# Optimization experiments

Measured on AMD Instinct MI355X. Metric: run time of the kernel, lower is better.

## Reference

```python
import jax, jax.numpy as jnp
import numpy as np

B, S, H = 2, 2048, 2048
NH, NKV, HD = 16, 4, 128
GROUPS = NH // NKV
THETA = 10000.0
EPS = 1e-6


def setup_inputs() -> dict:
    key = jax.random.key(0)
    ks = jax.random.split(key, 6)
    scale = 0.02
    return {
        "hidden_states": jax.random.normal(ks[0], (B, S, H), jnp.float32),
        "wq": jax.random.normal(ks[1], (NH * HD, H), jnp.float32) * scale,
        "wk": jax.random.normal(ks[2], (NKV * HD, H), jnp.float32) * scale,
        "wv": jax.random.normal(ks[3], (NKV * HD, H), jnp.float32) * scale,
        "wo": jax.random.normal(ks[4], (H, NH * HD), jnp.float32) * scale,
        "q_norm_weight": jnp.ones((HD,), jnp.float32),
        "k_norm_weight": jnp.ones((HD,), jnp.float32),
    }


def _rope_tables(seq_len):
    inv_freq = 1.0 / (THETA ** (jnp.arange(0, HD, 2, dtype=jnp.float32) / HD))
    t = jnp.arange(seq_len, dtype=jnp.float32)
    freqs = jnp.outer(t, inv_freq)              # [S, HD/2]
    emb = jnp.concatenate([freqs, freqs], -1)   # [S, HD]
    return jnp.cos(emb), jnp.sin(emb)


def _rotate_half(x):
    x1, x2 = x[..., : HD // 2], x[..., HD // 2:]
    return jnp.concatenate([-x2, x1], -1)


def _rmsnorm(x, w):
    var = jnp.mean(jnp.square(x), axis=-1, keepdims=True)
    return x * jax.lax.rsqrt(var + EPS) * w


def reference(hidden_states, wq, wk, wv, wo, q_norm_weight, k_norm_weight):
    b, s, _ = hidden_states.shape
    q = (hidden_states @ wq.T).reshape(b, s, NH, HD).transpose(0, 2, 1, 3)    # [b,nh,s,d]
    k = (hidden_states @ wk.T).reshape(b, s, NKV, HD).transpose(0, 2, 1, 3)   # [b,nkv,s,d]
    v = (hidden_states @ wv.T).reshape(b, s, NKV, HD).transpose(0, 2, 1, 3)

    cos, sin = _rope_tables(s)                  # [s,d]
    q = q * cos + _rotate_half(q) * sin
    k = k * cos + _rotate_half(k) * sin

    # fused QK RMSNorm (applied inside fused_qknorm_flash_attention)
    q = _rmsnorm(q, q_norm_weight)
    k = _rmsnorm(k, k_norm_weight)

    # GQA: share each kv head across GROUPS query heads without materializing repeats
    qg = q.reshape(b, NKV, GROUPS, s, HD)
    scale = 1.0 / jnp.sqrt(jnp.float32(HD))
    scores = jnp.einsum('bhgqd,bhkd->bhgqk', qg, k) * scale   # [b,nkv,g,s,s]
    causal = jnp.tril(jnp.ones((s, s), bool))
    scores = jnp.where(causal, scores, jnp.finfo(scores.dtype).min)
    probs = jax.nn.softmax(scores, axis=-1)
    out = jnp.einsum('bhgqk,bhkd->bhgqd', probs, v)            # [b,nkv,g,s,d]
    out = out.reshape(b, NH, s, HD).transpose(0, 2, 1, 3).reshape(b, s, NH * HD)
    return out @ wo.T
```

## Files before the change

### kernel.cpp

```cpp
#include <hip/hip_runtime.h>
#include <math.h>

typedef __bf16 bf16;
typedef __bf16 bf16x8 __attribute__((ext_vector_type(8)));
typedef __bf16 bf16x4 __attribute__((ext_vector_type(4)));
typedef float f32x4 __attribute__((ext_vector_type(4)));
typedef unsigned int u32;

#define B_DIM 2
#define S_LEN 2048
#define H_DIM 2048
#define NH 16
#define NKV 4
#define HD 128

__device__ __forceinline__ void gl_lds16(const void* g, void* l) {
    __builtin_amdgcn_global_load_lds(
        (const __attribute__((address_space(1))) unsigned int*)g,
        (__attribute__((address_space(3))) unsigned int*)l, 16, 0, 0);
}

__device__ __forceinline__ void bar() {
    asm volatile("" ::: "memory");
    __builtin_amdgcn_s_barrier();
    asm volatile("" ::: "memory");
}

__global__ __launch_bounds__(256) void cast_all(const float* __restrict__ s0,
                                                const float* __restrict__ s1,
                                                const float* __restrict__ s2,
                                                const float* __restrict__ s3,
                                                const float* __restrict__ s4,
                                                bf16* __restrict__ dst) {
    const int i = blockIdx.x * 256 + threadIdx.x;
    const float* src;
    int off;
    if (i < 2097152)      { src = s0; off = 0; }
    else if (i < 3145728) { src = s1; off = 2097152; }
    else if (i < 3407872) { src = s2; off = 3145728; }
    else if (i < 3670016) { src = s3; off = 3407872; }
    else                  { src = s4; off = 3670016; }
    float4 f = ((const float4*)src)[i - off];
    bf16x4 o = { (bf16)f.x, (bf16)f.y, (bf16)f.z, (bf16)f.w };
    *(bf16x4*)(dst + (size_t)i * 4) = o;
}

template <typename OutT>
__global__ __launch_bounds__(512, 2) void gemm256(const bf16* __restrict__ A,
                                                  const bf16* __restrict__ Bt,
                                                  OutT* __restrict__ C,
                                                  int M, int N, int K) {
    __shared__ __align__(16) bf16 smem[65536];
    const int t = threadIdx.x, lane = t & 63, w = t >> 6;
    const int lr = lane & 15, quad = lane >> 4;
    const int nN = N >> 8;
    const int nwg = gridDim.x, chunk = nwg >> 3;
    const int bid = blockIdx.x;
    const int lid = (bid & 7) * chunk + (bid >> 3);
    const int m0 = (lid / nN) << 8, n0 = (lid % nN) << 8;
    const int mh_w = w >> 2;
    const int wn = (w & 3) << 6;
    const int nh_w = (w & 3) >> 1;
    const int rb = (w & 1) << 6;
    const int nK = K >> 6;

    const int ld0 = w * 2;
    const int lrow = lane >> 2;
    const int csrc = (lane & 3) ^ ((lane >> 3) & 3);
    const int swz = (lr >> 1) & 3;

    auto stA = [&](int ts, int mh) {
        if (ts < nK) {
            bf16* db = smem + (ts & 1) * 16384 + mh * 8192;
            const bf16* sp = A + (size_t)(m0 + mh * 128) * K + ts * 64;
#pragma unroll
            for (int i = 0; i < 2; i++) {
                const int ldi = ld0 + i, kb = ldi >> 3, rg = ldi & 7;
                gl_lds16(sp + (size_t)(rg * 16 + lrow) * K + kb * 32 + csrc * 8,
                         db + kb * 4096 + rg * 512);
            }
        }
    };
    auto stB = [&](int ts, int nh) {
        if (ts < nK) {
            bf16* db = smem + 32768 + (ts & 1) * 16384 + nh * 8192;
            const bf16* sp = Bt + (size_t)(n0 + nh * 128) * K + ts * 64;
#pragma unroll
            for (int i = 0; i < 2; i++) {
                const int ldi = ld0 + i, kb = ldi >> 3, rg = ldi & 7;
                gl_lds16(sp + (size_t)(rg * 16 + lrow) * K + kb * 32 + csrc * 8,
                         db + kb * 4096 + rg * 512);
            }
        }
    };

    f32x4 acc[8][4];
#pragma unroll
    for (int i = 0; i < 8; i++)
#pragma unroll
        for (int j = 0; j < 4; j++) acc[i][j] = (f32x4){0.f, 0.f, 0.f, 0.f};
    bf16x8 af[8], b0[4], b1[4];

    auto rdA = [&](int s, int fi0) {
        const bf16* bp = smem + s * 16384 + mh_w * 8192;
#pragma unroll
        for (int f = 0; f < 4; f++)
#pragma unroll
            for (int ks = 0; ks < 2; ks++)
                af[f * 2 + ks] = *(const bf16x8*)(bp + ks * 4096 +
                                                  ((fi0 + f) * 16 + lr) * 32 + (quad ^ swz) * 8);
    };
    auto rdB = [&](int s, int fj0, bf16x8* dst) {
        const bf16* bp = smem + 32768 + s * 16384 + nh_w * 8192;
#pragma unroll
        for (int f = 0; f < 2; f++)
#pragma unroll
            for (int ks = 0; ks < 2; ks++)
                dst[f * 2 + ks] = *(const bf16x8*)(bp + ks * 4096 +
                                                   (rb + (fj0 + f) * 16 + lr) * 32 + (quad ^ swz) * 8);
    };
    auto mm16 = [&](int fi0, int fj0, bf16x8* bb) {
        __builtin_amdgcn_s_setprio(1);
#pragma unroll
        for (int f = 0; f < 4; f++)
#pragma unroll
            for (int g = 0; g < 2; g++)
#pragma unroll
                for (int ks = 0; ks < 2; ks++)
                    acc[fi0 + f][fj0 + g] = __builtin_amdgcn_mfma_f32_16x16x32_bf16(
                        af[f * 2 + ks], bb[g * 2 + ks], acc[fi0 + f][fj0 + g], 0, 0, 0);
        __builtin_amdgcn_s_setprio(0);
    };

    stA(0, 0); stA(0, 1); stB(0, 0); stB(0, 1); stA(1, 0);
    asm volatile("s_waitcnt vmcnt(2)" ::: "memory");
    bar();

    for (int ts = 0; ts < nK; ++ts) {
        const int s = ts & 1;
        rdA(s, 0); rdB(s, 0, b0);
        stA(ts + 1, 1);
        bar();
        mm16(0, 0, b0);
        bar();
        rdB(s, 2, b1);
        stB(ts + 1, 0);
        bar();
        mm16(0, 2, b1);
        bar();
        rdA(s, 4);
        stB(ts + 1, 1);
        bar();
        mm16(4, 2, b1);
        bar();
        rdB(s, 0, b0);
        stA(ts + 2, 0);
        bar();
        mm16(4, 0, b0);
        if (ts + 2 < nK) asm volatile("s_waitcnt vmcnt(2)" ::: "memory");
        else             asm volatile("s_waitcnt vmcnt(0)" ::: "memory");
        bar();
    }
#pragma unroll
    for (int fi = 0; fi < 8; fi++) {
        const int m = m0 + mh_w * 128 + fi * 16 + quad * 4;
#pragma unroll
        for (int fj = 0; fj < 4; fj++) {
            const int n = n0 + wn + fj * 16 + lr;
#pragma unroll
            for (int r = 0; r < 4; r++)
                C[(size_t)(m + r) * N + n] = (OutT)acc[fi][fj][r];
        }
    }
}

__global__ __launch_bounds__(512, 1) void gemm_pn(const bf16* __restrict__ A,
                                                  const bf16* __restrict__ Bt,
                                                  float* __restrict__ C,
                                                  int M, int N, int K) {
    __shared__ __align__(16) bf16 smem[49152];
    const int t = threadIdx.x, lane = t & 63, w = t >> 6;
    const int lr = lane & 15, quad = lane >> 4;
    const int nN = N >> 7;
    const int nwg = gridDim.x, chunk = nwg >> 3;
    const int bid = blockIdx.x;
    const int lid = (bid & 7) * chunk + (bid >> 3);
    const int m0 = (lid / nN) << 8, n0 = (lid % nN) << 7;
    const int mh_w = w >> 2;
    const int wn = (w & 3) << 5;
    const int nK = K >> 6;

    const int ld0 = w * 2;
    const int lrow = lane >> 2;
    const int csrc = (lane & 3) ^ ((lane >> 3) & 3);
    const int swz = (lr >> 1) & 3;

    auto stA = [&](int ts, int mh) {
        if (ts < nK) {
            bf16* db = smem + (ts & 1) * 16384 + mh * 8192;
            const bf16* sp = A + (size_t)(m0 + mh * 128) * K + ts * 64;
#pragma unroll
            for (int i = 0; i < 2; i++) {
                const int ldi = ld0 + i, kb = ldi >> 3, rg = ldi & 7;
                gl_lds16(sp + (size_t)(rg * 16 + lrow) * K + kb * 32 + csrc * 8,
                         db + kb * 4096 + rg * 512);
            }
        }
    };
    auto stB1 = [&](int ts) {
        if (ts < nK) {
            bf16* db = smem + 32768 + (ts & 1) * 8192;
            const bf16* sp = Bt + (size_t)n0 * K + ts * 64;
#pragma unroll
            for (int i = 0; i < 2; i++) {
                const int ldi = ld0 + i, kb = ldi >> 3, rg = ldi & 7;
                gl_lds16(sp + (size_t)(rg * 16 + lrow) * K + kb * 32 + csrc * 8,
                         db + kb * 4096 + rg * 512);
            }
        }
    };

    f32x4 acc[8][2];
#pragma unroll
    for (int i = 0; i < 8; i++)
#pragma unroll
        for (int j = 0; j < 2; j++) acc[i][j] = (f32x4){0.f, 0.f, 0.f, 0.f};
    bf16x8 af[8], bf1[4];

    auto rdA = [&](int s, int fi0) {
        const bf16* bp = smem + s * 16384 + mh_w * 8192;
#pragma unroll
        for (int f = 0; f < 4; f++)
#pragma unroll
            for (int ks = 0; ks < 2; ks++)
                af[f * 2 + ks] = *(const bf16x8*)(bp + ks * 4096 +
                                                  ((fi0 + f) * 16 + lr) * 32 + (quad ^ swz) * 8);
    };
    auto rdB1 = [&](int s) {
        const bf16* bp = smem + 32768 + s * 8192;
#pragma unroll
        for (int f = 0; f < 2; f++)
#pragma unroll
            for (int ks = 0; ks < 2; ks++)
                bf1[f * 2 + ks] = *(const bf16x8*)(bp + ks * 4096 +
                                                   (wn + f * 16 + lr) * 32 + (quad ^ swz) * 8);
    };
    auto mm8 = [&](int fi0, int ks) {
        __builtin_amdgcn_s_setprio(1);
#pragma unroll
        for (int f = 0; f < 4; f++)
#pragma unroll
            for (int g = 0; g < 2; g++)
                acc[fi0 + f][g] = __builtin_amdgcn_mfma_f32_16x16x32_bf16(
                    af[f * 2 + ks], bf1[g * 2 + ks], acc[fi0 + f][g], 0, 0, 0);
        __builtin_amdgcn_s_setprio(0);
    };

    stA(0, 0); stA(0, 1); stB1(0);
    asm volatile("s_waitcnt vmcnt(0)" ::: "memory");
    bar();

    for (int ts = 0; ts < nK; ++ts) {
        const int s = ts & 1;
        rdA(s, 0); rdB1(s);
        stA(ts + 1, 0);
        bar();
        mm8(0, 0);
        bar();
        stA(ts + 1, 1);
        stB1(ts + 1);
        bar();
        mm8(0, 1);
        bar();
        rdA(s, 4);
        bar();
        mm8(4, 0);
        bar();
        mm8(4, 1);
        asm volatile("s_waitcnt vmcnt(0)" ::: "memory");
        bar();
    }
#pragma unroll
    for (int fi = 0; fi < 8; fi++) {
        const int m = m0 + mh_w * 128 + fi * 16 + quad * 4;
#pragma unroll
        for (int fj = 0; fj < 2; fj++) {
            const int n = n0 + wn + fj * 16 + lr;
#pragma unroll
            for (int r = 0; r < 4; r++)
                C[(size_t)(m + r) * N + n] = acc[fi][fj][r];
        }
    }
}

__global__ __launch_bounds__(256) void rope_rms(const bf16* __restrict__ qkv,
                                                const float* __restrict__ qw,
                                                const float* __restrict__ kw,
                                                bf16* __restrict__ qb,
                                                bf16* __restrict__ kb,
                                                bf16* __restrict__ vt) {
    const int tok = blockIdx.x;
    const int b = tok >> 11, s = tok & (S_LEN - 1);
    const int lane = threadIdx.x & 63, w = threadIdx.x >> 6;
    const bf16* row = qkv + (size_t)tok * 3072;
    const float inv = expf(-(float)lane * (9.210340371976184f / 64.f));
    const float ang = (float)s * inv;
    float s_, c_;
    sincosf(ang, &s_, &c_);
    const float wq1 = qw[lane], wq2 = qw[lane + 64];
    const float wk1 = kw[lane], wk2 = kw[lane + 64];
    for (int u = w; u < 24; u += 4) {
        if (u < 16) {
            const float x1 = (float)row[u * 128 + lane], x2 = (float)row[u * 128 + 64 + lane];
            float y1 = x1 * c_ - x2 * s_;
            float y2 = x2 * c_ + x1 * s_;
            float ss = y1 * y1 + y2 * y2;
#pragma unroll
            for (int m = 1; m < 64; m <<= 1) ss += __shfl_xor(ss, m);
            const float r = rsqrtf(ss * (1.f / 128.f) + 1e-6f);
            size_t o = ((size_t)(b * NH + u) * S_LEN + s) * HD;
            qb[o + lane]      = (bf16)(y1 * r * wq1);
            qb[o + 64 + lane] = (bf16)(y2 * r * wq2);
        } else if (u < 20) {
            const int kh = u - 16;
            const float x1 = (float)row[2048 + kh * 128 + lane], x2 = (float)row[2048 + kh * 128 + 64 + lane];
            float y1 = x1 * c_ - x2 * s_;
            float y2 = x2 * c_ + x1 * s_;
            float ss = y1 * y1 + y2 * y2;
#pragma unroll
            for (int m = 1; m < 64; m <<= 1) ss += __shfl_xor(ss, m);
            const float r = rsqrtf(ss * (1.f / 128.f) + 1e-6f);
            size_t base = (size_t)(b * NKV + kh) * 16 * 16384;
            kb[base + (size_t)(lane >> 3) * 16384 + s * 8 + (lane & 7)]       = (bf16)(y1 * r * wk1);
            kb[base + (size_t)(8 + (lane >> 3)) * 16384 + s * 8 + (lane & 7)] = (bf16)(y2 * r * wk2);
        } else {
            const int vh = u - 20;
            const float x1 = (float)row[2560 + vh * 128 + lane], x2 = (float)row[2560 + vh * 128 + 64 + lane];
            const int m = s & 31;
            const int gi = (s >> 5) * 4 + ((m & 15) >> 2);
            const int el = ((m >> 4) << 2) | (m & 3);
            size_t base = ((size_t)(b * NKV + vh) * 256 + gi) * 1024 + el;
            vt[base + (size_t)lane * 8]        = (bf16)x1;
            vt[base + (size_t)(lane + 64) * 8] = (bf16)x2;
        }
    }
}

__global__ __launch_bounds__(256, 2) void flash(const bf16* __restrict__ qg,
                                                const bf16* __restrict__ kg,
                                                const bf16* __restrict__ vg,
                                                bf16* __restrict__ attn,
                                                float* __restrict__ part_o,
                                                float* __restrict__ part_l) {
    static const unsigned char QT[22] = {9,8,15,15,7,14,14,13,13,6,12,12,11,11,5,10,10,4,3,2,1,0};
    static const unsigned char CK[22] = {2,2,0,1,2,0,1,0,1,2,0,1,0,1,2,0,1,2,2,2,2,2};
    const int idx = blockIdx.x;
    const int g = idx >> 5, hb = idx & 31;
    const int qt = QT[g], ck = CK[g];
    const int h = hb & 15, b = hb >> 4;
    const int kvh = h >> 2;
    const int ktBeg = (ck == 1) ? (qt + 1) : 0;
    const int ktEnd = (ck == 0) ? (qt + 1) : (2 * qt + 2);
    const bf16* qh = qg + (size_t)(b * NH + h) * S_LEN * HD;
    const bf16* kh = kg + (size_t)(b * NKV + kvh) * (16 * 16384);
    const bf16* vh = vg + (size_t)(b * NKV + kvh) * (256 * 1024);
    __shared__ __align__(16) bf16 Ks[2][16 * 512];
    __shared__ __align__(16) bf16 Vs[2][8 * 1024];
    const int t = threadIdx.x, lane = t & 63, w = t >> 6, lr = lane & 15, quad = lane >> 4;
    const int row0 = qt * 128 + w * 32;
    bf16x8 qf[2][4];
#pragma unroll
    for (int mg = 0; mg < 2; mg++)
#pragma unroll
        for (int c = 0; c < 4; c++)
            qf[mg][c] = *(const bf16x8*)(qh + (size_t)(row0 + mg * 16 + lr) * HD + c * 32 + quad * 8);
    f32x4 o[2][8];
    f32x4 lacc[2];
#pragma unroll
    for (int mg = 0; mg < 2; mg++) {
        lacc[mg] = (f32x4){0.f, 0.f, 0.f, 0.f};
#pragma unroll
        for (int j = 0; j < 8; j++) o[mg][j] = (f32x4){0.f, 0.f, 0.f, 0.f};
    }
    const bf16 one = (bf16)1.0f;
    const bf16x8 ones8 = {one, one, one, one, one, one, one, one};
    const float C1 = 0.12751744f;
    const float C2 = -17.3123405f;

    const bf16* kp[4];
    const bf16* vp[2];
#pragma unroll
    for (int i = 0; i < 4; i++) kp[i] = kh + (size_t)(w * 4 + i) * 16384 + lane * 8;
#pragma unroll
    for (int i = 0; i < 2; i++) vp[i] = vh + (size_t)(w * 2 + i) * 1024 + lane * 8;

    auto stage = [&](int kt_, int bi) {
        const size_t kb8 = (size_t)kt_ * 512;
#pragma unroll
        for (int i = 0; i < 4; i++)
            gl_lds16(kp[i] + kb8, &Ks[bi][(w * 4 + i) * 512]);
        const size_t vb = (size_t)kt_ * 8192;
#pragma unroll
        for (int i = 0; i < 2; i++) {
            gl_lds16(vp[i] + vb, &Vs[bi][(w * 2 + i) * 1024]);
            gl_lds16(vp[i] + vb + 512, &Vs[bi][(w * 2 + i) * 1024 + 512]);
        }
    };

    stage(ktBeg, 0);
    __syncthreads();
    int cur = 0;

    for (int kt = ktBeg; kt < ktEnd; ++kt) {
        const int kbase = kt * 64;
        if (kt + 1 < ktEnd) stage(kt + 1, cur ^ 1);
        f32x4 sacc[2][4];
#pragma unroll
        for (int mg = 0; mg < 2; mg++)
#pragma unroll
            for (int n = 0; n < 4; n++) sacc[mg][n] = (f32x4){0.f, 0.f, 0.f, 0.f};
        __builtin_amdgcn_s_setprio(1);
#pragma unroll
        for (int c = 0; c < 4; c++)
#pragma unroll
            for (int n = 0; n < 4; n++) {
                bf16x8 kf = *(const bf16x8*)&Ks[cur][(c * 4 + quad) * 512 + (n * 16 + lr) * 8];
                sacc[0][n] = __builtin_amdgcn_mfma_f32_16x16x32_bf16(kf, qf[0][c], sacc[0][n], 0, 0, 0);
                sacc[1][n] = __builtin_amdgcn_mfma_f32_16x16x32_bf16(kf, qf[1][c], sacc[1][n], 0, 0, 0);
            }
        __builtin_amdgcn_s_setprio(0);
        const bool diag = (kt >= 2 * qt);
        u32 pw[2][8];
#pragma unroll
        for (int mg = 0; mg < 2; mg++) {
            const int qrow = row0 + mg * 16 + lr;
#pragma unroll
            for (int n = 0; n < 4; n++) {
                float e0, e1, e2, e3;
                {
                    float ev0 = exp2f(fmaf(sacc[mg][n][0], C1, C2));
                    float ev1 = exp2f(fmaf(sacc[mg][n][1], C1, C2));
                    float ev2 = exp2f(fmaf(sacc[mg][n][2], C1, C2));
                    float ev3 = exp2f(fmaf(sacc[mg][n][3], C1, C2));
                    if (diag) {
                        const int key = kbase + n * 16 + quad * 4;
                        ev0 = (key + 0 <= qrow) ? ev0 : 0.f;
                        ev1 = (key + 1 <= qrow) ? ev1 : 0.f;
                        ev2 = (key + 2 <= qrow) ? ev2 : 0.f;
                        ev3 = (key + 3 <= qrow) ? ev3 : 0.f;
                    }
                    e0 = ev0; e1 = ev1; e2 = ev2; e3 = ev3;
                }
                asm("v_cvt_pk_bf16_f32 %0, %1, %2"
                    : "=v"(pw[mg][(n >> 1) * 4 + (n & 1) * 2 + 0]) : "v"(e0), "v"(e1));
                asm("v_cvt_pk_bf16_f32 %0, %1, %2"
                    : "=v"(pw[mg][(n >> 1) * 4 + (n & 1) * 2 + 1]) : "v"(e2), "v"(e3));
            }
        }
        __builtin_amdgcn_s_setprio(1);
#pragma unroll
        for (int k2 = 0; k2 < 2; k2++) {
            const bf16x8 p0 = *(const bf16x8*)&pw[0][k2 * 4];
            const bf16x8 p1 = *(const bf16x8*)&pw[1][k2 * 4];
#pragma unroll
            for (int j = 0; j < 8; j++) {
                bf16x8 vf = *(const bf16x8*)&Vs[cur][(k2 * 4 + quad) * 1024 + (j * 16 + lr) * 8];
                o[0][j] = __builtin_amdgcn_mfma_f32_16x16x32_bf16(vf, p0, o[0][j], 0, 0, 0);
                o[1][j] = __builtin_amdgcn_mfma_f32_16x16x32_bf16(vf, p1, o[1][j], 0, 0, 0);
            }
            lacc[0] = __builtin_amdgcn_mfma_f32_16x16x32_bf16(ones8, p0, lacc[0], 0, 0, 0);
            lacc[1] = __builtin_amdgcn_mfma_f32_16x16x32_bf16(ones8, p1, lacc[1], 0, 0, 0);
        }
        __builtin_amdgcn_s_setprio(0);
        __syncthreads();
        cur ^= 1;
    }
    if (ck == 2) {
#pragma unroll
        for (int mg = 0; mg < 2; mg++) {
            const float inv = 1.0f / lacc[mg][0];
            const int qrow = row0 + mg * 16 + lr;
            bf16* dst = attn + ((size_t)(b * S_LEN) + qrow) * (NH * HD) + h * HD + quad * 4;
#pragma unroll
            for (int j = 0; j < 8; j++) {
                bf16x4 st = { (bf16)(o[mg][j][0] * inv), (bf16)(o[mg][j][1] * inv),
                              (bf16)(o[mg][j][2] * inv), (bf16)(o[mg][j][3] * inv) };
                *(bf16x4*)(dst + j * 16) = st;
            }
        }
    } else {
        const int slot = ((b * NH + h) * 6 + (qt - 10)) * 2 + ck;
        float* po = part_o + (size_t)slot * 16384;
#pragma unroll
        for (int mg = 0; mg < 2; mg++) {
            const int row = w * 32 + mg * 16 + lr;
#pragma unroll
            for (int j = 0; j < 8; j++) {
                float4 st = { o[mg][j][0], o[mg][j][1], o[mg][j][2], o[mg][j][3] };
                *(float4*)(po + row * 128 + j * 16 + quad * 4) = st;
            }
            if (quad == 0) part_l[slot * 128 + row] = lacc[mg][0];
        }
    }
}

__global__ __launch_bounds__(256) void reduce_attn(const float* __restrict__ part_o,
                                                   const float* __restrict__ part_l,
                                                   bf16* __restrict__ attn) {
    const int blk = blockIdx.x;
    const int qt = (blk % 6) + 10;
    const int h = (blk / 6) & 15, b = blk / 96;
    const float* p0 = part_o + (size_t)(blk * 2 + 0) * 16384;
    const float* p1 = part_o + (size_t)(blk * 2 + 1) * 16384;
    const float* l0 = part_l + (blk * 2 + 0) * 128;
    const float* l1 = part_l + (blk * 2 + 1) * 128;
    const int t = threadIdx.x;
#pragma unroll
    for (int it = 0; it < 16; it++) {
        const int idx = it * 256 + t;
        const int row = idx >> 5, d4 = idx & 31;
        float4 a = ((const float4*)p0)[idx];
        float4 c = ((const float4*)p1)[idx];
        const float inv = 1.0f / (l0[row] + l1[row]);
        bf16x4 ov = { (bf16)((a.x + c.x) * inv), (bf16)((a.y + c.y) * inv),
                      (bf16)((a.z + c.z) * inv), (bf16)((a.w + c.w) * inv) };
        *(bf16x4*)(attn + ((size_t)(b * S_LEN) + qt * 128 + row) * (NH * HD) + h * HD + d4 * 4) = ov;
    }
}

extern "C" void kernel_launch(void* const* d_in, const int* in_sizes, int n_in,
                              void* d_out, int out_size, void* d_ws, size_t ws_size,
                              hipStream_t stream) {
    (void)in_sizes; (void)n_in; (void)out_size; (void)ws_size;
    const float* hs  = (const float*)d_in[0];
    const float* wq  = (const float*)d_in[1];
    const float* wk  = (const float*)d_in[2];
    const float* wv  = (const float*)d_in[3];
    const float* wo  = (const float*)d_in[4];
    const float* qnw = (const float*)d_in[5];
    const float* knw = (const float*)d_in[6];
    float* out = (float*)d_out;

    char* ws = (char*)d_ws;
    size_t off = 0;
    auto alloc = [&](size_t bytes) {
        void* p = ws + off;
        off += (bytes + 255) & ~(size_t)255;
        return p;
    };
    bf16* hs_bf   = (bf16*)alloc((size_t)4096 * 2048 * 2);
    bf16* wqkv_bf = (bf16*)alloc((size_t)3072 * 2048 * 2);
    bf16* wo_bf   = (bf16*)alloc((size_t)2048 * 2048 * 2);
    bf16* qkv_bf  = (bf16*)alloc((size_t)4096 * 3072 * 2);
    bf16* q_bf    = (bf16*)alloc((size_t)B_DIM * NH * S_LEN * HD * 2);
    bf16* k_bf    = (bf16*)alloc((size_t)B_DIM * NKV * S_LEN * HD * 2);
    bf16* vt_bf   = (bf16*)alloc((size_t)B_DIM * NKV * S_LEN * HD * 2);
    bf16* at_bf   = (bf16*)alloc((size_t)4096 * 2048 * 2);

    float* part_o = (float*)hs_bf;
    float* part_l = (float*)((char*)hs_bf + (size_t)384 * 16384 * 4);

    cast_all<<<18432, 256, 0, stream>>>(hs, wq, wk, wv, wo, hs_bf);
    gemm256<bf16><<<dim3(192), 512, 0, stream>>>(hs_bf, wqkv_bf, qkv_bf, 4096, 3072, 2048);
    rope_rms<<<4096, 256, 0, stream>>>(qkv_bf, qnw, knw, q_bf, k_bf, vt_bf);
    flash<<<dim3(704), 256, 0, stream>>>(q_bf, k_bf, vt_bf, at_bf, part_o, part_l);
    reduce_attn<<<dim3(192), 256, 0, stream>>>(part_o, part_l, at_bf);
    gemm_pn<<<dim3(256), 512, 0, stream>>>(at_bf, wo_bf, out, 4096, 2048, 2048);
}
```

Measured before the change: 302.8 us.

## Split flash attention Q tile across eight waves of 16 rows each

The flash kernel now launches 512 threads per block, and each of the eight waves owns 16 query rows instead of four waves owning 32 rows each. Per-wave register state (Q fragments, output accumulators, score tiles) is halved, and the K/V staging work is spread over more waves. The goal is higher occupancy and more latency hiding. In exchange, each K/V fragment read from LDS now feeds one MFMA instead of two, which doubles LDS read traffic per FLOP, and there are more waves at each barrier.

Result: no change. 303.3 us (+0.2%).

```diff
diff --git a/kernel.cpp b/kernel.cpp
--- a/kernel.cpp
+++ b/kernel.cpp
@@ -346,7 +346,7 @@
     }
 }
 
-__global__ __launch_bounds__(256, 2) void flash(const bf16* __restrict__ qg,
+__global__ __launch_bounds__(512, 4) void flash(const bf16* __restrict__ qg,
                                                 const bf16* __restrict__ kg,
                                                 const bf16* __restrict__ vg,
                                                 bf16* __restrict__ attn,
@@ -367,44 +367,33 @@
     __shared__ __align__(16) bf16 Ks[2][16 * 512];
     __shared__ __align__(16) bf16 Vs[2][8 * 1024];
     const int t = threadIdx.x, lane = t & 63, w = t >> 6, lr = lane & 15, quad = lane >> 4;
-    const int row0 = qt * 128 + w * 32;
-    bf16x8 qf[2][4];
-#pragma unroll
-    for (int mg = 0; mg < 2; mg++)
-#pragma unroll
-        for (int c = 0; c < 4; c++)
-            qf[mg][c] = *(const bf16x8*)(qh + (size_t)(row0 + mg * 16 + lr) * HD + c * 32 + quad * 8);
-    f32x4 o[2][8];
-    f32x4 lacc[2];
-#pragma unroll
-    for (int mg = 0; mg < 2; mg++) {
-        lacc[mg] = (f32x4){0.f, 0.f, 0.f, 0.f};
-#pragma unroll
-        for (int j = 0; j < 8; j++) o[mg][j] = (f32x4){0.f, 0.f, 0.f, 0.f};
-    }
+    const int row0 = qt * 128 + w * 16;
+    bf16x8 qf[4];
+#pragma unroll
+    for (int c = 0; c < 4; c++)
+        qf[c] = *(const bf16x8*)(qh + (size_t)(row0 + lr) * HD + c * 32 + quad * 8);
+    f32x4 o[8];
+    f32x4 lacc = (f32x4){0.f, 0.f, 0.f, 0.f};
+#pragma unroll
+    for (int j = 0; j < 8; j++) o[j] = (f32x4){0.f, 0.f, 0.f, 0.f};
     const bf16 one = (bf16)1.0f;
     const bf16x8 ones8 = {one, one, one, one, one, one, one, one};
     const float C1 = 0.12751744f;
     const float C2 = -17.3123405f;
 
-    const bf16* kp[4];
-    const bf16* vp[2];
-#pragma unroll
-    for (int i = 0; i < 4; i++) kp[i] = kh + (size_t)(w * 4 + i) * 16384 + lane * 8;
-#pragma unroll
-    for (int i = 0; i < 2; i++) vp[i] = vh + (size_t)(w * 2 + i) * 1024 + lane * 8;
+    const bf16* kp[2];
+#pragma unroll
+    for (int i = 0; i < 2; i++) kp[i] = kh + (size_t)(w * 2 + i) * 16384 + lane * 8;
+    const bf16* vp = vh + (size_t)w * 1024 + lane * 8;
 
     auto stage = [&](int kt_, int bi) {
         const size_t kb8 = (size_t)kt_ * 512;
 #pragma unroll
-        for (int i = 0; i < 4; i++)
-            gl_lds16(kp[i] + kb8, &Ks[bi][(w * 4 + i) * 512]);
+        for (int i = 0; i < 2; i++)
+            gl_lds16(kp[i] + kb8, &Ks[bi][(w * 2 + i) * 512]);
         const size_t vb = (size_t)kt_ * 8192;
-#pragma unroll
-        for (int i = 0; i < 2; i++) {
-            gl_lds16(vp[i] + vb, &Vs[bi][(w * 2 + i) * 1024]);
-            gl_lds16(vp[i] + vb + 512, &Vs[bi][(w * 2 + i) * 1024 + 512]);
-        }
+        gl_lds16(vp + vb, &Vs[bi][w * 1024]);
+        gl_lds16(vp + vb + 512, &Vs[bi][w * 1024 + 512]);
     };
 
     stage(ktBeg, 0);
@@ -414,34 +403,30 @@
     for (int kt = ktBeg; kt < ktEnd; ++kt) {
         const int kbase = kt * 64;
         if (kt + 1 < ktEnd) stage(kt + 1, cur ^ 1);
-        f32x4 sacc[2][4];
-#pragma unroll
-        for (int mg = 0; mg < 2; mg++)
-#pragma unroll
-            for (int n = 0; n < 4; n++) sacc[mg][n] = (f32x4){0.f, 0.f, 0.f, 0.f};
+        f32x4 sacc[4];
+#pragma unroll
+        for (int n = 0; n < 4; n++) sacc[n] = (f32x4){0.f, 0.f, 0.f, 0.f};
         __builtin_amdgcn_s_setprio(1);
 #pragma unroll
         for (int c = 0; c < 4; c++)
 #pragma unroll
             for (int n = 0; n < 4; n++) {
                 bf16x8 kf = *(const bf16x8*)&Ks[cur][(c * 4 + quad) * 512 + (n * 16 + lr) * 8];
-                sacc[0][n] = __builtin_amdgcn_mfma_f32_16x16x32_bf16(kf, qf[0][c], sacc[0][n], 0, 0, 0);
-                sacc[1][n] = __builtin_amdgcn_mfma_f32_16x16x32_bf16(kf, qf[1][c], sacc[1][n], 0, 0, 0);
+                sacc[n] = __builtin_amdgcn_mfma_f32_16x16x32_bf16(kf, qf[c], sacc[n], 0, 0, 0);
             }
         __builtin_amdgcn_s_setprio(0);
         const bool diag = (kt >= 2 * qt);
-        u32 pw[2][8];
-#pragma unroll
-        for (int mg = 0; mg < 2; mg++) {
-            const int qrow = row0 + mg * 16 + lr;
+        u32 pw[8];
+        {
+            const int qrow = row0 + lr;
 #pragma unroll
             for (int n = 0; n < 4; n++) {
                 float e0, e1, e2, e3;
                 {
-                    float ev0 = exp2f(fmaf(sacc[mg][n][0], C1, C2));
-                    float ev1 = exp2f(fmaf(sacc[mg][n][1], C1, C2));
-                    float ev2 = exp2f(fmaf(sacc[mg][n][2], C1, C2));
-                    float ev3 = exp2f(fmaf(sacc[mg][n][3], C1, C2));
+                    float ev0 = exp2f(fmaf(sacc[n][0], C1, C2));
+                    float ev1 = exp2f(fmaf(sacc[n][1], C1, C2));
+                    float ev2 = exp2f(fmaf(sacc[n][2], C1, C2));
+                    float ev3 = exp2f(fmaf(sacc[n][3], C1, C2));
                     if (diag) {
                         const int key = kbase + n * 16 + quad * 4;
                         ev0 = (key + 0 <= qrow) ? ev0 : 0.f;
@@ -452,55 +437,46 @@
                     e0 = ev0; e1 = ev1; e2 = ev2; e3 = ev3;
                 }
                 asm("v_cvt_pk_bf16_f32 %0, %1, %2"
-                    : "=v"(pw[mg][(n >> 1) * 4 + (n & 1) * 2 + 0]) : "v"(e0), "v"(e1));
+                    : "=v"(pw[(n >> 1) * 4 + (n & 1) * 2 + 0]) : "v"(e0), "v"(e1));
                 asm("v_cvt_pk_bf16_f32 %0, %1, %2"
-                    : "=v"(pw[mg][(n >> 1) * 4 + (n & 1) * 2 + 1]) : "v"(e2), "v"(e3));
+                    : "=v"(pw[(n >> 1) * 4 + (n & 1) * 2 + 1]) : "v"(e2), "v"(e3));
             }
         }
         __builtin_amdgcn_s_setprio(1);
 #pragma unroll
         for (int k2 = 0; k2 < 2; k2++) {
-            const bf16x8 p0 = *(const bf16x8*)&pw[0][k2 * 4];
-            const bf16x8 p1 = *(const bf16x8*)&pw[1][k2 * 4];
+            const bf16x8 p0 = *(const bf16x8*)&pw[k2 * 4];
 #pragma unroll
             for (int j = 0; j < 8; j++) {
                 bf16x8 vf = *(const bf16x8*)&Vs[cur][(k2 * 4 + quad) * 1024 + (j * 16 + lr) * 8];
-                o[0][j] = __builtin_amdgcn_mfma_f32_16x16x32_bf16(vf, p0, o[0][j], 0, 0, 0);
-                o[1][j] = __builtin_amdgcn_mfma_f32_16x16x32_bf16(vf, p1, o[1][j], 0, 0, 0);
-            }
-            lacc[0] = __builtin_amdgcn_mfma_f32_16x16x32_bf16(ones8, p0, lacc[0], 0, 0, 0);
-            lacc[1] = __builtin_amdgcn_mfma_f32_16x16x32_bf16(ones8, p1, lacc[1], 0, 0, 0);
+                o[j] = __builtin_amdgcn_mfma_f32_16x16x32_bf16(vf, p0, o[j], 0, 0, 0);
+            }
+            lacc = __builtin_amdgcn_mfma_f32_16x16x32_bf16(ones8, p0, lacc, 0, 0, 0);
         }
         __builtin_amdgcn_s_setprio(0);
         __syncthreads();
         cur ^= 1;
     }
     if (ck == 2) {
-#pragma unroll
-        for (int mg = 0; mg < 2; mg++) {
-            const float inv = 1.0f / lacc[mg][0];
-            const int qrow = row0 + mg * 16 + lr;
-            bf16* dst = attn + ((size_t)(b * S_LEN) + qrow) * (NH * HD) + h * HD + quad * 4;
-#pragma unroll
-            for (int j = 0; j < 8; j++) {
-                bf16x4 st = { (bf16)(o[mg][j][0] * inv), (bf16)(o[mg][j][1] * inv),
-                              (bf16)(o[mg][j][2] * inv), (bf16)(o[mg][j][3] * inv) };
-                *(bf16x4*)(dst + j * 16) = st;
-            }
+        const float inv = 1.0f / lacc[0];
+        const int qrow = row0 + lr;
+        bf16* dst = attn + ((size_t)(b * S_LEN) + qrow) * (NH * HD) + h * HD + quad * 4;
+#pragma unroll
+        for (int j = 0; j < 8; j++) {
+            bf16x4 st = { (bf16)(o[j][0] * inv), (bf16)(o[j][1] * inv),
+                          (bf16)(o[j][2] * inv), (bf16)(o[j][3] * inv) };
+            *(bf16x4*)(dst + j * 16) = st;
         }
     } else {
         const int slot = ((b * NH + h) * 6 + (qt - 10)) * 2 + ck;
         float* po = part_o + (size_t)slot * 16384;
-#pragma unroll
-        for (int mg = 0; mg < 2; mg++) {
-            const int row = w * 32 + mg * 16 + lr;
-#pragma unroll
-            for (int j = 0; j < 8; j++) {
-                float4 st = { o[mg][j][0], o[mg][j][1], o[mg][j][2], o[mg][j][3] };
-                *(float4*)(po + row * 128 + j * 16 + quad * 4) = st;
-            }
-            if (quad == 0) part_l[slot * 128 + row] = lacc[mg][0];
-        }
+        const int row = w * 16 + lr;
+#pragma unroll
+        for (int j = 0; j < 8; j++) {
+            float4 st = { o[j][0], o[j][1], o[j][2], o[j][3] };
+            *(float4*)(po + row * 128 + j * 16 + quad * 4) = st;
+        }
+        if (quad == 0) part_l[slot * 128 + row] = lacc[0];
     }
 }
 
@@ -563,7 +539,7 @@
     cast_all<<<18432, 256, 0, stream>>>(hs, wq, wk, wv, wo, hs_bf);
     gemm256<bf16><<<dim3(192), 512, 0, stream>>>(hs_bf, wqkv_bf, qkv_bf, 4096, 3072, 2048);
     rope_rms<<<4096, 256, 0, stream>>>(qkv_bf, qnw, knw, q_bf, k_bf, vt_bf);
-    flash<<<dim3(704), 256, 0, stream>>>(q_bf, k_bf, vt_bf, at_bf, part_o, part_l);
+    flash<<<dim3(704), 512, 0, stream>>>(q_bf, k_bf, vt_bf, at_bf, part_o, part_l);
     reduce_attn<<<dim3(192), 256, 0, stream>>>(part_o, part_l, at_bf);
     gemm_pn<<<dim3(256), 512, 0, stream>>>(at_bf, wo_bf, out, 4096, 2048, 2048);
 }
```
